# Performance work log

Measured on AMD Instinct MI355X. Metric: run time of the kernel, lower is better.

Reference implementation:

```python
import jax, jax.numpy as jnp
import numpy as np
import math

KH, KW = 3, 3
CIN, COUT = 48, 48
H, W = 128, 128
DELTA = 0.001


def _gabor_weights(freq, theta, sigma, psi, f0, theta0):
    # grids exactly as in torch __init__: x0 = ceil(kh/2), linspace(-x0+1, x0, kh)
    x0 = math.ceil(KH / 2)
    y0 = math.ceil(KW / 2)
    ly = jnp.linspace(-x0 + 1.0, float(x0), KH)
    lx = jnp.linspace(-y0 + 1.0, float(y0), KW)
    Y, X = jnp.meshgrid(ly, lx, indexing='ij')  # [kh,kw], Y varies on dim0
    # broadcast per-(out,in) scalars over the kernel grid -> [O,I,kh,kw]
    th = theta[:, :, None, None]
    sg = sigma[:, :, None, None]
    fr = freq[:, :, None, None]
    ps = psi[:, :, None, None]
    F0 = f0[:, :, None, None]
    th0 = theta0[:, :, None, None]
    rotx = X * jnp.cos(th) + Y * jnp.sin(th)
    roty = -X * jnp.sin(th) + Y * jnp.cos(th)
    r = jnp.sqrt(rotx ** 2 + roty ** 2 + DELTA)
    g_radial = jnp.exp(-((jnp.log(r) - jnp.log(F0)) / (2.0 * jnp.log(sg / F0))) ** 2)
    g_angular = jnp.exp(-(th - th0) ** 2 / (2.0 * sg ** 2))
    g = g_radial * g_angular * jnp.cos(fr * r + ps)
    g = g / (2.0 * math.pi * sg ** 2)
    return g  # [O,I,KH,KW]


def setup_inputs() -> dict:
    key = jax.random.key(0)
    ks = jax.random.split(key, 5)
    pi = math.pi
    return {
        'x': jax.random.normal(ks[0], (1, CIN, H, W), dtype=jnp.float32),
        'freq': jax.random.uniform(ks[1], (COUT, CIN), dtype=jnp.float32) * pi,
        'theta': jax.random.uniform(ks[2], (COUT, CIN), dtype=jnp.float32) * pi,
        'sigma': jax.random.uniform(ks[3], (COUT, CIN), dtype=jnp.float32) * pi,
        'psi': jax.random.uniform(ks[4], (COUT, CIN), dtype=jnp.float32) * pi,
        'f0': jnp.ones((COUT, CIN), dtype=jnp.float32),
        'theta0': jnp.ones((COUT, CIN), dtype=jnp.float32),
    }


def reference(x, freq, theta, sigma, psi, f0, theta0):
    w = _gabor_weights(freq, theta, sigma, psi, f0, theta0)  # [O,I,kh,kw]
    # frequency-domain filtering: fft2(x) [1,I,H,W] * fft2(w, s=(H,W)) [O,I,H,W]
    x_freq = jnp.fft.fft2(x)
    w_freq = jnp.fft.fft2(w, s=(H, W))
    xf = x_freq * w_freq  # broadcast (B=1) -> [O,I,H,W]
    crow, ccol = H // 2, W // 2
    mask = jnp.zeros((H, W), dtype=x.dtype).at[crow - 30:crow + 30, ccol - 30:ccol + 30].set(1.0)
    x_filtered = jnp.fft.ifft2(xf * mask).real  # [O,I,H,W]
    out = jax.lax.conv_general_dilated(
        x_filtered, w,
        window_strides=(1, 1), padding=[(1, 1), (1, 1)],
        dimension_numbers=('NCHW', 'OIHW', 'NCHW'))
    return out  # [O,O,H,W]
```

## Files before the change

kernel.cpp:

```cpp
#include <hip/hip_runtime.h>

#define CIN 48
#define COUT 48
#define NPIX 16384
#define XFP 52

typedef float f32x4 __attribute__((ext_vector_type(4)));
typedef short bf16x8 __attribute__((ext_vector_type(8)));

__device__ __forceinline__ unsigned short f2bf(float f) {
  unsigned u = __float_as_uint(f);
  unsigned r = (u + 0x7FFFu + ((u >> 16) & 1u)) >> 16;
  return (unsigned short)r;
}

__global__ __launch_bounds__(256) void gabor_k(
    const float* __restrict__ freq, const float* __restrict__ theta,
    const float* __restrict__ sigma, const float* __restrict__ psi,
    const float* __restrict__ f0, const float* __restrict__ theta0,
    float* __restrict__ wout, unsigned short* __restrict__ wbf64)
{
  int idx = blockIdx.x * 256 + threadIdx.x;
  if (idx < 432 * 16) {
    wbf64[(idx >> 4) * 64 + 48 + (idx & 15)] = 0;
  }
  if (idx >= COUT * CIN * 9) return;
  int k = idx % 9;
  int oi = idx / 9;
  int oc = oi / CIN, ic = oi % CIN;
  int a = k / 3, b = k % 3;
  float Yv = (a == 0) ? -1.0f : ((a == 1) ? 0.5f : 2.0f);
  float Xv = (b == 0) ? -1.0f : ((b == 1) ? 0.5f : 2.0f);
  float th = theta[oi], sg = sigma[oi], fr = freq[oi], ps = psi[oi];
  float F0 = f0[oi], th0 = theta0[oi];
  float c = cosf(th), s = sinf(th);
  float rotx =  Xv * c + Yv * s;
  float roty = -Xv * s + Yv * c;
  float r = sqrtf(rotx * rotx + roty * roty + 0.001f);
  float denom = 2.0f * logf(sg / F0);
  float t1 = (logf(r) - logf(F0)) / denom;
  float g_rad = expf(-t1 * t1);
  float dth = th - th0;
  float g_ang = expf(-dth * dth / (2.0f * sg * sg));
  float g = g_rad * g_ang * cosf(fr * r + ps) / (6.283185307179586f * sg * sg);
  wout[idx] = g;
  wbf64[(k * 48 + oc) * 64 + ic] = f2bf(g);
}

__global__ void circ_k(float* __restrict__ ar, float* __restrict__ ai)
{
  int d = threadIdx.x;
  float sr = 0.f, si = 0.f;
  for (int u = 34; u < 94; ++u) {
    int m = (u * d) & 127;
    float ang = (float)m * 0.049087385212340526f;
    sr += cosf(ang);
    si += sinf(ang);
  }
  ar[d] = sr * (1.0f / 128.0f);
  ai[d] = si * (1.0f / 128.0f);
}

__global__ __launch_bounds__(256) void stage1_k(
    const float* __restrict__ x, const float* __restrict__ arr,
    const float* __restrict__ aii, float2* __restrict__ Up)
{
  __shared__ float Xs[16 * 128];
  __shared__ float ars[128], ais[128];
  int yg = blockIdx.x, i = blockIdx.y;
  int t = threadIdx.x;
  const float* Xi = x + i * NPIX + yg * 16 * 128;
  for (int p = t; p < 2048; p += 256) Xs[p] = Xi[p];
  if (t < 128) { ars[t] = arr[t]; ais[t] = aii[t]; }
  __syncthreads();
  int j = t & 127;
  int ysl = t >> 7;
  float accr[8], acci[8];
#pragma unroll
  for (int yy = 0; yy < 8; ++yy) { accr[yy] = 0.f; acci[yy] = 0.f; }
  for (int xx = 0; xx < 128; ++xx) {
    float tr = ars[(j - xx) & 127];
    float ti = ais[(j - xx) & 127];
#pragma unroll
    for (int yy = 0; yy < 8; ++yy) {
      float xv = Xs[(ysl * 8 + yy) * 128 + xx];
      accr[yy] += xv * tr;
      acci[yy] += xv * ti;
    }
  }
  float2* UpI = Up + i * NPIX;
  int ybase = yg * 16 + ysl * 8;
#pragma unroll
  for (int yy = 0; yy < 8; ++yy)
    UpI[(ybase + yy) * 128 + j] = make_float2(accr[yy], acci[yy]);
}

__global__ __launch_bounds__(256) void stage2_k(
    const float2* __restrict__ Up, const float* __restrict__ arr,
    const float* __restrict__ aii, float* __restrict__ yf)
{
  __shared__ float2 Us[128 * 16];
  __shared__ float ars[128], ais[128];
  int jg = blockIdx.x, i = blockIdx.y;
  int t = threadIdx.x;
  const float2* UpI = Up + i * NPIX;
  for (int p = t; p < 2048; p += 256) {
    int y = p >> 4, jj = p & 15;
    Us[p] = UpI[y * 128 + jg * 16 + jj];
  }
  if (t < 128) { ars[t] = arr[t]; ais[t] = aii[t]; }
  __syncthreads();
  int yp = t & 127;
  int xsl = t >> 7;
  float acc[8];
#pragma unroll
  for (int xx = 0; xx < 8; ++xx) acc[xx] = 0.f;
  for (int y = 0; y < 128; ++y) {
    float tr = ars[(yp - y) & 127];
    float ti = ais[(yp - y) & 127];
#pragma unroll
    for (int xx = 0; xx < 8; ++xx) {
      float2 u = Us[y * 16 + xsl * 8 + xx];
      acc[xx] += u.x * tr - u.y * ti;
    }
  }
  float* yfI = yf + i * NPIX;
  int xb = jg * 16 + xsl * 8;
#pragma unroll
  for (int xx = 0; xx < 8; ++xx)
    yfI[yp * 128 + xb + xx] = acc[xx];
}

__global__ __launch_bounds__(256, 3) void conv2_k(
    const float* __restrict__ yf, const float* __restrict__ wts,
    const unsigned short* __restrict__ wbf64, float* __restrict__ out)
{
  __shared__ __align__(16) short XF[324 * XFP + 16];

  int o  = blockIdx.z;
  int y0 = blockIdx.y * 16, x0 = blockIdx.x * 16;
  int tid = threadIdx.x;

  for (int p = tid; p < 324; p += 256)
    *(uint2*)(XF + p * XFP + 48) = make_uint2(0u, 0u);
  if (tid < 16) XF[324 * XFP + tid] = 0;

  if (tid < 240) {
    int sA = tid, sB = tid + 240;
    int iA = sA / 10, rA = sA - iA * 10, spA = rA % 5, hA = rA / 5;
    int iB = sB / 10, rB = sB - iB * 10, spB = rB % 5, hB = rB / 5;
    const float* WpA = wts + (o * CIN + iA) * 9;
    const float* WpB = wts + (o * CIN + iB) * 9;
    float WA0 = WpA[0], WA1 = WpA[1], WA2 = WpA[2], WA3 = WpA[3], WA4 = WpA[4],
          WA5 = WpA[5], WA6 = WpA[6], WA7 = WpA[7], WA8 = WpA[8];
    float WB0 = WpB[0], WB1 = WpB[1], WB2 = WpB[2], WB3 = WpB[3], WB4 = WpB[4],
          WB5 = WpB[5], WB6 = WpB[6], WB7 = WpB[7], WB8 = WpB[8];
    const float* yfA = yf + iA * NPIX;
    const float* yfB = yf + iB * NPIX;
    int cbA = (x0 - 4 + 4 * spA) & 127;
    int cbB = (x0 - 4 + 4 * spB) & 127;
    int rbA = hA * 9, rbB = hB * 9;
    float RaA[8], RbA[8], RcA[8], RaB[8], RbB[8], RcB[8];

#define LOADA(dst, ry) { \
    const float* rp_ = yfA + (((ry) & 127) << 7); \
    float4 q0_ = *(const float4*)(rp_ + cbA); \
    float4 q1_ = *(const float4*)(rp_ + ((cbA + 4) & 127)); \
    dst[0]=q0_.x; dst[1]=q0_.y; dst[2]=q0_.z; dst[3]=q0_.w; \
    dst[4]=q1_.x; dst[5]=q1_.y; dst[6]=q1_.z; dst[7]=q1_.w; }
#define LOADB(dst, ry) { \
    const float* rp_ = yfB + (((ry) & 127) << 7); \
    float4 q0_ = *(const float4*)(rp_ + cbB); \
    float4 q1_ = *(const float4*)(rp_ + ((cbB + 4) & 127)); \
    dst[0]=q0_.x; dst[1]=q0_.y; dst[2]=q0_.z; dst[3]=q0_.w; \
    dst[4]=q1_.x; dst[5]=q1_.y; dst[6]=q1_.z; dst[7]=q1_.w; }

#define EMITA(rr, R2_, R1_, R0_) { \
    int y_ = y0 - 1 + (rr); \
    bool yok_ = (y_ >= 0) && (y_ < 128); \
    _Pragma("unroll") \
    for (int j = 0; j < 4; ++j) { \
      int cidx_ = 4 * spA + j; \
      if (cidx_ < 18) { \
        int xg_ = x0 - 1 + cidx_; \
        float v_ = 0.f; \
        if (yok_ && xg_ >= 0 && xg_ < 128) { \
          v_ = WA0 * R0_[j + 3] + WA1 * R0_[j + 2] + WA2 * R0_[j + 1] \
             + WA3 * R1_[j + 3] + WA4 * R1_[j + 2] + WA5 * R1_[j + 1] \
             + WA6 * R2_[j + 3] + WA7 * R2_[j + 2] + WA8 * R2_[j + 1]; \
        } \
        XF[((rr) * 18 + cidx_) * XFP + iA] = (short)f2bf(v_); \
      } } }
#define EMITB(rr, R2_, R1_, R0_) { \
    int y_ = y0 - 1 + (rr); \
    bool yok_ = (y_ >= 0) && (y_ < 128); \
    _Pragma("unroll") \
    for (int j = 0; j < 4; ++j) { \
      int cidx_ = 4 * spB + j; \
      if (cidx_ < 18) { \
        int xg_ = x0 - 1 + cidx_; \
        float v_ = 0.f; \
        if (yok_ && xg_ >= 0 && xg_ < 128) { \
          v_ = WB0 * R0_[j + 3] + WB1 * R0_[j + 2] + WB2 * R0_[j + 1] \
             + WB3 * R1_[j + 3] + WB4 * R1_[j + 2] + WB5 * R1_[j + 1] \
             + WB6 * R2_[j + 3] + WB7 * R2_[j + 2] + WB8 * R2_[j + 1]; \
        } \
        XF[((rr) * 18 + cidx_) * XFP + iB] = (short)f2bf(v_); \
      } } }

    LOADA(RaA, y0 - 3 + rbA)  LOADB(RaB, y0 - 3 + rbB)
    LOADA(RbA, y0 - 2 + rbA)  LOADB(RbB, y0 - 2 + rbB)
#pragma unroll
    for (int rr0 = 0; rr0 < 9; rr0 += 3) {
      LOADA(RcA, y0 - 1 + rbA + rr0)  LOADB(RcB, y0 - 1 + rbB + rr0)
      EMITA(rbA + rr0,     RaA, RbA, RcA)  EMITB(rbB + rr0,     RaB, RbB, RcB)
      LOADA(RaA, y0 + rbA + rr0)      LOADB(RaB, y0 + rbB + rr0)
      EMITA(rbA + rr0 + 1, RbA, RcA, RaA)  EMITB(rbB + rr0 + 1, RbB, RcB, RaB)
      LOADA(RbA, y0 + 1 + rbA + rr0)  LOADB(RbB, y0 + 1 + rbB + rr0)
      EMITA(rbA + rr0 + 2, RcA, RaA, RbA)  EMITB(rbB + rr0 + 2, RcB, RaB, RbB)
    }
#undef LOADA
#undef LOADB
#undef EMITA
#undef EMITB
  }
  __syncthreads();

  int wv = tid >> 6, lane = tid & 63;
  int tx = lane & 15, gq = lane >> 4;
  f32x4 acc[4][3];
#pragma unroll
  for (int nn = 0; nn < 4; ++nn)
#pragma unroll
    for (int m = 0; m < 3; ++m) acc[nn][m] = (f32x4){0.f, 0.f, 0.f, 0.f};

  const unsigned short* abase = wbf64 + (tx)*64;

  for (int k = 0; k < 9; ++k) {
    bf16x8 Ac0[3], Ac1[3];
#pragma unroll
    for (int m = 0; m < 3; ++m) {
      const unsigned short* ap = abase + (k * 48 + m * 16) * 64;
      Ac0[m] = *(const bf16x8*)(ap + gq * 8);
      Ac1[m] = *(const bf16x8*)(ap + 32 + gq * 8);
    }
    int dy = k / 3, dx = k - dy * 3;
#pragma unroll
    for (int nn = 0; nn < 4; ++nn) {
      int n = wv * 4 + nn;
      const short* bp = XF + ((n + dy) * 18 + tx + dx) * XFP;
      bf16x8 B0 = *(const bf16x8*)(bp + gq * 8);
      bf16x8 B1 = *(const bf16x8*)(bp + 32 + gq * 8);
#pragma unroll
      for (int m = 0; m < 3; ++m) {
        acc[nn][m] = __builtin_amdgcn_mfma_f32_16x16x32_bf16(Ac0[m], B0, acc[nn][m], 0, 0, 0);
        acc[nn][m] = __builtin_amdgcn_mfma_f32_16x16x32_bf16(Ac1[m], B1, acc[nn][m], 0, 0, 0);
      }
    }
  }

#pragma unroll
  for (int nn = 0; nn < 4; ++nn) {
    int y = y0 + wv * 4 + nn;
#pragma unroll
    for (int m = 0; m < 3; ++m) {
#pragma unroll
      for (int r = 0; r < 4; ++r) {
        int oc = m * 16 + gq * 4 + r;
        out[((size_t)(o * COUT + oc) << 14) + (y << 7) + x0 + tx] = acc[nn][m][r];
      }
    }
  }
}

extern "C" void kernel_launch(void* const* d_in, const int* in_sizes, int n_in,
                              void* d_out, int out_size, void* d_ws, size_t ws_size,
                              hipStream_t stream)
{
  const float* x      = (const float*)d_in[0];
  const float* freq   = (const float*)d_in[1];
  const float* theta  = (const float*)d_in[2];
  const float* sigma  = (const float*)d_in[3];
  const float* psi    = (const float*)d_in[4];
  const float* f0     = (const float*)d_in[5];
  const float* theta0 = (const float*)d_in[6];
  float* out = (float*)d_out;
  float* ws  = (float*)d_ws;

  float*  w   = ws;
  float*  ar  = ws + 20736;
  float*  ai  = ws + 20864;
  float2* Up  = (float2*)(ws + 21248);
  float*  yf  = ws + 21248 + CIN * NPIX * 2;
  unsigned short* wbf64 = (unsigned short*)(ws + 21248 + CIN * NPIX * 3);

  gabor_k<<<dim3(81), dim3(256), 0, stream>>>(freq, theta, sigma, psi, f0, theta0, w, wbf64);
  circ_k<<<dim3(1), dim3(128), 0, stream>>>(ar, ai);
  stage1_k<<<dim3(8, 48), dim3(256), 0, stream>>>(x, ar, ai, Up);
  stage2_k<<<dim3(8, 48), dim3(256), 0, stream>>>(Up, ar, ai, yf);
  conv2_k<<<dim3(8, 8, 48), dim3(256), 0, stream>>>(yf, w, wbf64, out);
}
```

Baseline: 174.2 us.

## Halve stage tiles, specialize interior conv tiles, prefetch MFMA A operands

```diff
diff --git a/kernel.cpp b/kernel.cpp
--- a/kernel.cpp
+++ b/kernel.cpp
@@ -13,6 +13,10 @@
   unsigned r = (u + 0x7FFFu + ((u >> 16) & 1u)) >> 16;
   return (unsigned short)r;
 }
+
+#define OFF_UP     21248
+#define OFF_YF     (OFF_UP + CIN * NPIX * 2)
+#define OFF_WBF64  (OFF_YF + CIN * NPIX)
 
 __global__ __launch_bounds__(256) void gabor_k(
     const float* __restrict__ freq, const float* __restrict__ theta,
@@ -65,33 +69,33 @@
     const float* __restrict__ x, const float* __restrict__ arr,
     const float* __restrict__ aii, float2* __restrict__ Up)
 {
-  __shared__ float Xs[16 * 128];
+  __shared__ float Xs[8 * 128];
   __shared__ float ars[128], ais[128];
   int yg = blockIdx.x, i = blockIdx.y;
   int t = threadIdx.x;
-  const float* Xi = x + i * NPIX + yg * 16 * 128;
-  for (int p = t; p < 2048; p += 256) Xs[p] = Xi[p];
+  const float* Xi = x + i * NPIX + yg * 8 * 128;
+  for (int p = t; p < 1024; p += 256) Xs[p] = Xi[p];
   if (t < 128) { ars[t] = arr[t]; ais[t] = aii[t]; }
   __syncthreads();
   int j = t & 127;
   int ysl = t >> 7;
-  float accr[8], acci[8];
-#pragma unroll
-  for (int yy = 0; yy < 8; ++yy) { accr[yy] = 0.f; acci[yy] = 0.f; }
+  float accr[4], acci[4];
+#pragma unroll
+  for (int yy = 0; yy < 4; ++yy) { accr[yy] = 0.f; acci[yy] = 0.f; }
   for (int xx = 0; xx < 128; ++xx) {
     float tr = ars[(j - xx) & 127];
     float ti = ais[(j - xx) & 127];
 #pragma unroll
-    for (int yy = 0; yy < 8; ++yy) {
-      float xv = Xs[(ysl * 8 + yy) * 128 + xx];
+    for (int yy = 0; yy < 4; ++yy) {
+      float xv = Xs[(ysl * 4 + yy) * 128 + xx];
       accr[yy] += xv * tr;
       acci[yy] += xv * ti;
     }
   }
   float2* UpI = Up + i * NPIX;
-  int ybase = yg * 16 + ysl * 8;
-#pragma unroll
-  for (int yy = 0; yy < 8; ++yy)
+  int ybase = yg * 8 + ysl * 4;
+#pragma unroll
+  for (int yy = 0; yy < 4; ++yy)
     UpI[(ybase + yy) * 128 + j] = make_float2(accr[yy], acci[yy]);
 }
 
@@ -99,35 +103,35 @@
     const float2* __restrict__ Up, const float* __restrict__ arr,
     const float* __restrict__ aii, float* __restrict__ yf)
 {
-  __shared__ float2 Us[128 * 16];
+  __shared__ float2 Us[128 * 8];
   __shared__ float ars[128], ais[128];
   int jg = blockIdx.x, i = blockIdx.y;
   int t = threadIdx.x;
   const float2* UpI = Up + i * NPIX;
-  for (int p = t; p < 2048; p += 256) {
-    int y = p >> 4, jj = p & 15;
-    Us[p] = UpI[y * 128 + jg * 16 + jj];
+  for (int p = t; p < 1024; p += 256) {
+    int y = p >> 3, jj = p & 7;
+    Us[p] = UpI[y * 128 + jg * 8 + jj];
   }
   if (t < 128) { ars[t] = arr[t]; ais[t] = aii[t]; }
   __syncthreads();
   int yp = t & 127;
   int xsl = t >> 7;
-  float acc[8];
-#pragma unroll
-  for (int xx = 0; xx < 8; ++xx) acc[xx] = 0.f;
+  float acc[4];
+#pragma unroll
+  for (int xx = 0; xx < 4; ++xx) acc[xx] = 0.f;
   for (int y = 0; y < 128; ++y) {
     float tr = ars[(yp - y) & 127];
     float ti = ais[(yp - y) & 127];
 #pragma unroll
-    for (int xx = 0; xx < 8; ++xx) {
-      float2 u = Us[y * 16 + xsl * 8 + xx];
+    for (int xx = 0; xx < 4; ++xx) {
+      float2 u = Us[y * 8 + xsl * 4 + xx];
       acc[xx] += u.x * tr - u.y * ti;
     }
   }
   float* yfI = yf + i * NPIX;
-  int xb = jg * 16 + xsl * 8;
-#pragma unroll
-  for (int xx = 0; xx < 8; ++xx)
+  int xb = jg * 8 + xsl * 4;
+#pragma unroll
+  for (int xx = 0; xx < 4; ++xx)
     yfI[yp * 128 + xb + xx] = acc[xx];
 }
 
@@ -145,6 +149,7 @@
     *(uint2*)(XF + p * XFP + 48) = make_uint2(0u, 0u);
   if (tid < 16) XF[324 * XFP + tid] = 0;
 
+  bool inter = (y0 >= 16) && (y0 <= 96) && (x0 >= 16) && (x0 <= 96);
   if (tid < 240) {
     int sA = tid, sB = tid + 240;
     int iA = sA / 10, rA = sA - iA * 10, spA = rA % 5, hA = rA / 5;
@@ -175,54 +180,57 @@
     dst[0]=q0_.x; dst[1]=q0_.y; dst[2]=q0_.z; dst[3]=q0_.w; \
     dst[4]=q1_.x; dst[5]=q1_.y; dst[6]=q1_.z; dst[7]=q1_.w; }
 
-#define EMITA(rr, R2_, R1_, R0_) { \
+#define EMITA(rr, R2_, R1_, R0_, CHK) { \
     int y_ = y0 - 1 + (rr); \
-    bool yok_ = (y_ >= 0) && (y_ < 128); \
     _Pragma("unroll") \
     for (int j = 0; j < 4; ++j) { \
       int cidx_ = 4 * spA + j; \
       if (cidx_ < 18) { \
-        int xg_ = x0 - 1 + cidx_; \
-        float v_ = 0.f; \
-        if (yok_ && xg_ >= 0 && xg_ < 128) { \
-          v_ = WA0 * R0_[j + 3] + WA1 * R0_[j + 2] + WA2 * R0_[j + 1] \
-             + WA3 * R1_[j + 3] + WA4 * R1_[j + 2] + WA5 * R1_[j + 1] \
-             + WA6 * R2_[j + 3] + WA7 * R2_[j + 2] + WA8 * R2_[j + 1]; \
+        float v_ = WA0 * R0_[j + 3] + WA1 * R0_[j + 2] + WA2 * R0_[j + 1] \
+                 + WA3 * R1_[j + 3] + WA4 * R1_[j + 2] + WA5 * R1_[j + 1] \
+                 + WA6 * R2_[j + 3] + WA7 * R2_[j + 2] + WA8 * R2_[j + 1]; \
+        if (CHK) { \
+          int xg_ = x0 - 1 + cidx_; \
+          if (!((y_ >= 0) && (y_ < 128) && (xg_ >= 0) && (xg_ < 128))) v_ = 0.f; \
         } \
         XF[((rr) * 18 + cidx_) * XFP + iA] = (short)f2bf(v_); \
       } } }
-#define EMITB(rr, R2_, R1_, R0_) { \
+#define EMITB(rr, R2_, R1_, R0_, CHK) { \
     int y_ = y0 - 1 + (rr); \
-    bool yok_ = (y_ >= 0) && (y_ < 128); \
     _Pragma("unroll") \
     for (int j = 0; j < 4; ++j) { \
       int cidx_ = 4 * spB + j; \
       if (cidx_ < 18) { \
-        int xg_ = x0 - 1 + cidx_; \
-        float v_ = 0.f; \
-        if (yok_ && xg_ >= 0 && xg_ < 128) { \
-          v_ = WB0 * R0_[j + 3] + WB1 * R0_[j + 2] + WB2 * R0_[j + 1] \
-             + WB3 * R1_[j + 3] + WB4 * R1_[j + 2] + WB5 * R1_[j + 1] \
-             + WB6 * R2_[j + 3] + WB7 * R2_[j + 2] + WB8 * R2_[j + 1]; \
+        float v_ = WB0 * R0_[j + 3] + WB1 * R0_[j + 2] + WB2 * R0_[j + 1] \
+                 + WB3 * R1_[j + 3] + WB4 * R1_[j + 2] + WB5 * R1_[j + 1] \
+                 + WB6 * R2_[j + 3] + WB7 * R2_[j + 2] + WB8 * R2_[j + 1]; \
+        if (CHK) { \
+          int xg_ = x0 - 1 + cidx_; \
+          if (!((y_ >= 0) && (y_ < 128) && (xg_ >= 0) && (xg_ < 128))) v_ = 0.f; \
         } \
         XF[((rr) * 18 + cidx_) * XFP + iB] = (short)f2bf(v_); \
       } } }
 
-    LOADA(RaA, y0 - 3 + rbA)  LOADB(RaB, y0 - 3 + rbB)
-    LOADA(RbA, y0 - 2 + rbA)  LOADB(RbB, y0 - 2 + rbB)
-#pragma unroll
-    for (int rr0 = 0; rr0 < 9; rr0 += 3) {
-      LOADA(RcA, y0 - 1 + rbA + rr0)  LOADB(RcB, y0 - 1 + rbB + rr0)
-      EMITA(rbA + rr0,     RaA, RbA, RcA)  EMITB(rbB + rr0,     RaB, RbB, RcB)
-      LOADA(RaA, y0 + rbA + rr0)      LOADB(RaB, y0 + rbB + rr0)
-      EMITA(rbA + rr0 + 1, RbA, RcA, RaA)  EMITB(rbB + rr0 + 1, RbB, RcB, RaB)
-      LOADA(RbA, y0 + 1 + rbA + rr0)  LOADB(RbB, y0 + 1 + rbB + rr0)
-      EMITA(rbA + rr0 + 2, RcA, RaA, RbA)  EMITB(rbB + rr0 + 2, RcB, RaB, RbB)
-    }
+#define PH1LOOP(CHK) { \
+    LOADA(RaA, y0 - 3 + rbA)  LOADB(RaB, y0 - 3 + rbB) \
+    LOADA(RbA, y0 - 2 + rbA)  LOADB(RbB, y0 - 2 + rbB) \
+    _Pragma("unroll") \
+    for (int rr0 = 0; rr0 < 9; rr0 += 3) { \
+      LOADA(RcA, y0 - 1 + rbA + rr0)  LOADB(RcB, y0 - 1 + rbB + rr0) \
+      EMITA(rbA + rr0,     RaA, RbA, RcA, CHK)  EMITB(rbB + rr0,     RaB, RbB, RcB, CHK) \
+      LOADA(RaA, y0 + rbA + rr0)      LOADB(RaB, y0 + rbB + rr0) \
+      EMITA(rbA + rr0 + 1, RbA, RcA, RaA, CHK)  EMITB(rbB + rr0 + 1, RbB, RcB, RaB, CHK) \
+      LOADA(RbA, y0 + 1 + rbA + rr0)  LOADB(RbB, y0 + 1 + rbB + rr0) \
+      EMITA(rbA + rr0 + 2, RcA, RaA, RbA, CHK)  EMITB(rbB + rr0 + 2, RcB, RaB, RbB, CHK) \
+    } }
+
+    if (inter) PH1LOOP(0) else PH1LOOP(1)
+
 #undef LOADA
 #undef LOADB
 #undef EMITA
 #undef EMITB
+#undef PH1LOOP
   }
   __syncthreads();
 
@@ -235,14 +243,22 @@
     for (int m = 0; m < 3; ++m) acc[nn][m] = (f32x4){0.f, 0.f, 0.f, 0.f};
 
   const unsigned short* abase = wbf64 + (tx)*64;
+  bf16x8 Ac0[3], Ac1[3], An0[3], An1[3];
+#pragma unroll
+  for (int m = 0; m < 3; ++m) {
+    const unsigned short* ap = abase + (m * 16) * 64;
+    Ac0[m] = *(const bf16x8*)(ap + gq * 8);
+    Ac1[m] = *(const bf16x8*)(ap + 32 + gq * 8);
+  }
 
   for (int k = 0; k < 9; ++k) {
-    bf16x8 Ac0[3], Ac1[3];
-#pragma unroll
-    for (int m = 0; m < 3; ++m) {
-      const unsigned short* ap = abase + (k * 48 + m * 16) * 64;
-      Ac0[m] = *(const bf16x8*)(ap + gq * 8);
-      Ac1[m] = *(const bf16x8*)(ap + 32 + gq * 8);
+    if (k < 8) {
+#pragma unroll
+      for (int m = 0; m < 3; ++m) {
+        const unsigned short* ap = abase + ((k + 1) * 48 + m * 16) * 64;
+        An0[m] = *(const bf16x8*)(ap + gq * 8);
+        An1[m] = *(const bf16x8*)(ap + 32 + gq * 8);
+      }
     }
     int dy = k / 3, dx = k - dy * 3;
 #pragma unroll
@@ -257,6 +273,8 @@
         acc[nn][m] = __builtin_amdgcn_mfma_f32_16x16x32_bf16(Ac1[m], B1, acc[nn][m], 0, 0, 0);
       }
     }
+#pragma unroll
+    for (int m = 0; m < 3; ++m) { Ac0[m] = An0[m]; Ac1[m] = An1[m]; }
   }
 
 #pragma unroll
@@ -287,16 +305,16 @@
   float* out = (float*)d_out;
   float* ws  = (float*)d_ws;
 
-  float*  w   = ws;
-  float*  ar  = ws + 20736;
-  float*  ai  = ws + 20864;
-  float2* Up  = (float2*)(ws + 21248);
-  float*  yf  = ws + 21248 + CIN * NPIX * 2;
-  unsigned short* wbf64 = (unsigned short*)(ws + 21248 + CIN * NPIX * 3);
+  float*  w     = ws;
+  float*  ar    = ws + 20736;
+  float*  ai    = ws + 20864;
+  float2* Up    = (float2*)(ws + OFF_UP);
+  float*  yf    = ws + OFF_YF;
+  unsigned short* wbf64 = (unsigned short*)(ws + OFF_WBF64);
 
   gabor_k<<<dim3(81), dim3(256), 0, stream>>>(freq, theta, sigma, psi, f0, theta0, w, wbf64);
   circ_k<<<dim3(1), dim3(128), 0, stream>>>(ar, ai);
-  stage1_k<<<dim3(8, 48), dim3(256), 0, stream>>>(x, ar, ai, Up);
-  stage2_k<<<dim3(8, 48), dim3(256), 0, stream>>>(Up, ar, ai, yf);
+  stage1_k<<<dim3(16, 48), dim3(256), 0, stream>>>(x, ar, ai, Up);
+  stage2_k<<<dim3(16, 48), dim3(256), 0, stream>>>(Up, ar, ai, yf);
   conv2_k<<<dim3(8, 8, 48), dim3(256), 0, stream>>>(yf, w, wbf64, out);
 }
```

Result: faster. 159.2 us (-8.6%).
